# Performance work log

Measured on AMD Instinct MI355X. Metric: run time of the kernel, lower is better.

The kernel has to match this reference:

```python
import jax, jax.numpy as jnp
import numpy as np

DIM = 128
HOP = 2
NEIGH = [12, 2]  # neighbor_num per hop
ALPHA = 0.2      # leaky-relu slope
NUM_NODE = 50000
B, S = 128, 50
STDV = 1.0 / np.sqrt(DIM)


def _leaky(x):
    return jnp.where(x >= 0, x, ALPHA * x)


def _local_agg(h, adj, a_local):
    # h: [B,S,D], adj: [B,S,S] ints in 0..4, a_local: [4,D]
    a_in = h[:, :, None, :] * h[:, None, :, :]            # [B,S,S,D]
    e = _leaky(jnp.einsum('bijd,kd->kbij', a_in, a_local))  # [4,B,S,S]
    att = jnp.full(adj.shape, -9e15, dtype=h.dtype)
    for k in range(4):
        att = jnp.where(adj == k + 1, e[k], att)
    att = jax.nn.softmax(att, axis=-1)
    return jnp.einsum('bij,bjd->bid', att, h)


def _global_agg(self_v, neigh_v, extra_v, w1, w2, w3, bias):
    # self_v: [B,N,D], neigh_v: [B,N,K,D], extra_v: [B,N,D]
    a = _leaky(jnp.einsum('bnkd,de->bnke', extra_v[:, :, None, :] * neigh_v, w1))
    a = jnp.einsum('bnke,e->bnk', a, w2)
    a = jax.nn.softmax(a, axis=-1)
    agg = jnp.einsum('bnk,bnkd->bnd', a, neigh_v)
    out = jnp.concatenate([self_v, agg], axis=-1) @ w3 + bias
    return jax.nn.relu(out)


def setup_inputs() -> dict:
    key = jax.random.key(0)
    ks = jax.random.split(key, 12)
    u = lambda k, shp: jax.random.uniform(k, shp, jnp.float32, -STDV, STDV)
    return {
        'inputs': jax.random.randint(ks[0], (B, S), 0, NUM_NODE),
        'adj': jax.random.randint(ks[1], (B, S, S), 0, 5),
        'mask_item': jnp.ones((B, S), dtype=jnp.int32),
        'item': jax.random.randint(ks[2], (B, S), 0, NUM_NODE),
        'first_adj': jax.random.randint(ks[3], (B, S * NEIGH[0]), 0, NUM_NODE),
        'adj_all': jax.random.randint(ks[4], (NUM_NODE, 2), 0, NUM_NODE),
        'embedding': u(ks[5], (NUM_NODE, DIM)),
        'a_local': u(ks[6], (4, DIM)),
        'gw1': u(ks[7], (HOP, DIM, DIM)),
        'gw2': u(ks[8], (HOP, DIM)),
        'gw3': u(ks[9], (HOP, 2 * DIM, DIM)),
        'gbias': u(ks[10], (HOP, DIM)),
    }


def reference(inputs, adj, mask_item, item, first_adj, adj_all,
              embedding, a_local, gw1, gw2, gw3, gbias):
    b, s = inputs.shape
    h = embedding[inputs]                                  # [B,S,D]
    h_local = _local_agg(h, adj, a_local)

    m = mask_item.astype(embedding.dtype)[..., None]       # [B,S,1]
    item_emb = embedding[item] * m
    sum_item = jnp.sum(item_emb, 1) / jnp.sum(m, 1)        # [B,D]
    sess = sum_item[:, None, :]                            # [B,1,D]

    # multi-hop neighbor sampling
    neigh1 = first_adj.reshape(b, s * NEIGH[0])            # [B, 600]
    neigh2 = adj_all[neigh1.reshape(-1)].reshape(b, s * NEIGH[0] * NEIGH[1])  # [B,1200]
    ev = [embedding[inputs], embedding[neigh1], embedding[neigh2]]

    for n_hop in range(HOP):
        nxt = []
        for hop in range(HOP - n_hop):
            neigh_v = ev[hop + 1].reshape(b, -1, NEIGH[hop], DIM)
            extra_v = jnp.broadcast_to(sess, (b, ev[hop].shape[1], DIM))
            nxt.append(_global_agg(ev[hop], neigh_v, extra_v,
                                   gw1[n_hop], gw2[n_hop], gw3[n_hop], gbias[n_hop]))
        ev = nxt
    h_global = ev[0].reshape(b, s, DIM)

    # dropout is identity at eval
    return h_local + h_global
```

## Files before the change

kernel.cpp:

```cpp
#include <hip/hip_runtime.h>
#include <stdint.h>

typedef unsigned short ushort_t;
typedef __attribute__((ext_vector_type(8))) short bf16x8;
typedef __attribute__((ext_vector_type(4))) float f32x4;

#define B_   128
#define S_   50
#define D_   128
#define ALPHA_ 0.2f

__device__ __forceinline__ float bf2f(ushort_t u){
  return __uint_as_float(((uint32_t)u) << 16);
}
__device__ __forceinline__ ushort_t f2bf(float f){
  uint32_t x = __float_as_uint(f);
  x = (x + 0x7fffu + ((x >> 16) & 1u)) >> 16;
  return (ushort_t)x;
}
__device__ __forceinline__ float leaky(float x){ return x >= 0.f ? x : ALPHA_*x; }

__device__ __forceinline__ int detect_flag_block(const uint32_t* __restrict__ emb_raw){
  __shared__ int flg;
  if (threadIdx.x == 0){
    int ok = 1;
    for (int i = 0; i < 64; i++){
      uint32_t lo = emb_raw[i] & 0xffffu;
      uint32_t ex = (lo >> 7) & 0xFFu;
      if (!(lo == 0u || (ex >= 64u && ex <= 126u))) ok = 0;
    }
    flg = ok;
  }
  __syncthreads();
  return flg;
}

__global__ void cvt_all(const void* __restrict__ p0, const void* __restrict__ p1,
                        const void* __restrict__ p2, const void* __restrict__ p3,
                        const void* __restrict__ p4, const void* __restrict__ p5,
                        ushort_t* __restrict__ dst){
  int flag = detect_flag_block((const uint32_t*)p0);
  const int seg_end[6] = {6400000, 6400512, 6433280, 6433536, 6499072, 6499328};
  int base = (blockIdx.x*256 + threadIdx.x) * 4;
  if (base >= 6499328) return;
  int s = 0;
  while (base >= seg_end[s]) s++;
  int segbase = (s == 0) ? 0 : seg_end[s-1];
  const void* src = (s==0)?p0:(s==1)?p1:(s==2)?p2:(s==3)?p3:(s==4)?p4:p5;
  int off = base - segbase;
  union { ushort_t u[4]; uint2 d2; } o;
  if (flag){
    o.d2 = *(const uint2*)((const ushort_t*)src + off);
  } else {
    float4 v = *(const float4*)((const float*)src + off);
    o.u[0] = f2bf(v.x); o.u[1] = f2bf(v.y); o.u[2] = f2bf(v.z); o.u[3] = f2bf(v.w);
  }
  *(uint2*)(dst + base) = o.d2;
}

__global__ void prep_frags(const void* __restrict__ emb_raw,
                           const void* __restrict__ w1r, const void* __restrict__ w3r,
                           uint4* __restrict__ w1f, uint4* __restrict__ w3f){
  int flag = detect_flag_block((const uint32_t*)emb_raw);
  int id = blockIdx.x*256 + threadIdx.x;
  if (id >= 12288) return;
  if (id < 4096){
    int h = id >> 11, i = id & 2047;
    int kt = i >> 9, rem = i & 511, t = rem >> 6, ln = rem & 63;
    int q = ln >> 4, c = ln & 15;
    union { ushort_t u[8]; uint4 q4; } e;
    #pragma unroll
    for (int j = 0; j < 8; j++){
      int idx = h*16384 + (32*kt + q*8 + j)*128 + 16*t + c;
      e.u[j] = flag ? ((const ushort_t*)w1r)[idx] : f2bf(((const float*)w1r)[idx]);
    }
    w1f[h*2048 + i] = e.q4;
  } else {
    int id2 = id - 4096;
    int h = id2 >> 12, i = id2 & 4095;
    int kt = i >> 9, rem = i & 511, t = rem >> 6, ln = rem & 63;
    int q = ln >> 4, c = ln & 15;
    union { ushort_t u[8]; uint4 q4; } e;
    #pragma unroll
    for (int j = 0; j < 8; j++){
      int idx = h*32768 + (32*kt + q*8 + j)*128 + 16*t + c;
      e.u[j] = flag ? ((const ushort_t*)w3r)[idx] : f2bf(((const float*)w3r)[idx]);
    }
    w3f[h*4096 + i] = e.q4;
  }
}

__global__ __launch_bounds__(256) void sess_local(
    const int* __restrict__ inputs, const int* __restrict__ adj,
    const int* __restrict__ item, const int* __restrict__ mask,
    const ushort_t* __restrict__ emb, const ushort_t* __restrict__ alocb,
    ushort_t* __restrict__ sessb, ushort_t* __restrict__ hlb){
  int blk = blockIdx.x;
  int tid = threadIdx.x;
  if (blk >= 512){
    int b = (blk - 512)*2 + (tid >> 7);
    int d = tid & 127;
    float acc = 0.f, den = 0.f;
    for (int s = 0; s < S_; s++){
      float fm = (float)mask[b*S_ + s];
      int id = item[b*S_ + s];
      acc += fm * bf2f(emb[(size_t)id*D_ + d]);
      den += fm;
    }
    sessb[b*D_ + d] = f2bf(acc / den);
    return;
  }
  __shared__ ushort_t hS[64][136];
  __shared__ float    attS[16][68];
  __shared__ int      sids[64];
  int b  = blk >> 2;
  int mi = blk & 3;
  if (tid < 64) sids[tid] = (tid < S_) ? inputs[b*S_ + tid] : 0;
  __syncthreads();
  for (int idx = tid; idx < 64*16; idx += 256){
    int j = idx >> 4, ch = idx & 15;
    uint4 v = {0u, 0u, 0u, 0u};
    if (j < S_) v = *(const uint4*)(emb + (size_t)sids[j]*D_ + ch*8);
    *(uint4*)(&hS[j][ch*8]) = v;
  }
  for (int idx = tid; idx < 16*64; idx += 256)
    attS[idx >> 6][idx & 63] = -9.0e15f;
  __syncthreads();

  int lane = tid & 63, wv = tid >> 6;
  int q = lane >> 4, c = lane & 15;

  f32x4 Eacc[4];
  #pragma unroll
  for (int ni = 0; ni < 4; ni++) Eacc[ni] = (f32x4){0.f,0.f,0.f,0.f};
  #pragma unroll
  for (int kt = 0; kt < 4; kt++){
    uint4 av = *(const uint4*)(alocb + wv*D_ + kt*32 + q*8);
    const uint32_t* ap = (const uint32_t*)&av;
    uint4 hv = *(const uint4*)(&hS[mi*16 + c][kt*32 + q*8]);
    const uint32_t* hp = (const uint32_t*)&hv;
    union { ushort_t u[8]; bf16x8 v; } afr;
    #pragma unroll
    for (int p = 0; p < 4; p++){
      float x0 = __uint_as_float(hp[p] << 16)         * __uint_as_float(ap[p] << 16);
      float x1 = __uint_as_float(hp[p] & 0xffff0000u) * __uint_as_float(ap[p] & 0xffff0000u);
      afr.u[2*p]   = f2bf(x0);
      afr.u[2*p+1] = f2bf(x1);
    }
    #pragma unroll
    for (int ni = 0; ni < 4; ni++){
      union { uint4 q4; bf16x8 v; } bfr;
      bfr.q4 = *(const uint4*)(&hS[ni*16 + c][kt*32 + q*8]);
      Eacc[ni] = __builtin_amdgcn_mfma_f32_16x16x32_bf16(afr.v, bfr.v, Eacc[ni], 0,0,0);
    }
  }
  const int* adjb = adj + (size_t)b*S_*S_;
  #pragma unroll
  for (int ni = 0; ni < 4; ni++){
    int j = ni*16 + c;
    #pragma unroll
    for (int r = 0; r < 4; r++){
      int i = mi*16 + q*4 + r;
      if (i < S_ && j < S_){
        int kk = adjb[i*S_ + j];
        if (kk == wv + 1) attS[q*4 + r][j] = leaky(Eacc[ni][r]);
      }
    }
  }
  __syncthreads();
  if (tid < 16){
    int i = mi*16 + tid;
    if (i < S_){
      float mx = -__builtin_inff();
      for (int j = 0; j < S_; j++) mx = fmaxf(mx, attS[tid][j]);
      float s = 0.f;
      for (int j = 0; j < S_; j++){ float e = __expf(attS[tid][j] - mx); attS[tid][j] = e; s += e; }
      float inv = 1.f / s;
      for (int j = 0; j < S_; j++) attS[tid][j] *= inv;
      for (int j = S_; j < 64; j++) attS[tid][j] = 0.f;
    } else {
      for (int j = 0; j < 64; j++) attS[tid][j] = 0.f;
    }
  }
  __syncthreads();
  f32x4 Pacc[2];
  Pacc[0] = (f32x4){0.f,0.f,0.f,0.f};
  Pacc[1] = (f32x4){0.f,0.f,0.f,0.f};
  #pragma unroll
  for (int kt = 0; kt < 2; kt++){
    union { ushort_t u[8]; bf16x8 v; } afr;
    const float* arow = &attS[c][kt*32 + q*8];
    #pragma unroll
    for (int j = 0; j < 8; j++) afr.u[j] = f2bf(arow[j]);
    #pragma unroll
    for (int nn = 0; nn < 2; nn++){
      int ni = 2*wv + nn;
      union { ushort_t u[8]; bf16x8 v; } bfr;
      #pragma unroll
      for (int jj = 0; jj < 8; jj++)
        bfr.u[jj] = hS[kt*32 + q*8 + jj][ni*16 + c];
      Pacc[nn] = __builtin_amdgcn_mfma_f32_16x16x32_bf16(afr.v, bfr.v, Pacc[nn], 0,0,0);
    }
  }
  #pragma unroll
  for (int nn = 0; nn < 2; nn++){
    int d = (2*wv + nn)*16 + c;
    #pragma unroll
    for (int r = 0; r < 4; r++){
      int i = mi*16 + q*4 + r;
      if (i < S_) hlb[((size_t)b*S_ + i)*D_ + d] = f2bf(Pacc[nn][r]);
    }
  }
}

__global__ __launch_bounds__(256) void score_mfma_ab(
    const ushort_t* __restrict__ sessb, const ushort_t* __restrict__ emb,
    const int* __restrict__ neigh1, const int* __restrict__ adj_all,
    const uint4* __restrict__ w1f, const ushort_t* __restrict__ w2,
    float* __restrict__ score, int nA){
  __shared__ uint4 bfrag[2048];
  int tid = threadIdx.x;
  for (int i = tid; i < 2048; i += 256) bfrag[i] = w1f[i];
  __syncthreads();
  int lane = tid & 63, wave = tid >> 6;
  int m = lane & 15, q = lane >> 4;
  float w2v[8];
  #pragma unroll
  for (int t = 0; t < 8; t++) w2v[t] = bf2f(w2[16*t + m]);

  for (int it = 0; it < 2; it++){
    int row_base = blockIdx.x*128 + it*64 + wave*16;
    int row = row_base + m;
    const ushort_t* nrow; int b;
    if (row < nA){
      nrow = emb + (size_t)neigh1[row]*D_;
      b = row / 600;
    } else {
      int r2 = row - nA;
      nrow = emb + (size_t)adj_all[(size_t)neigh1[r2>>1]*2 + (r2&1)]*D_;
      b = r2 / 1200;
    }
    const ushort_t* srow = sessb + (size_t)b*D_;

    f32x4 acc[8];
    #pragma unroll
    for (int t = 0; t < 8; t++) acc[t] = (f32x4){0.f,0.f,0.f,0.f};
    #pragma unroll
    for (int kt = 0; kt < 4; kt++){
      uint4 nv = *(const uint4*)(nrow + kt*32 + q*8);
      uint4 sv = *(const uint4*)(srow + kt*32 + q*8);
      const uint32_t* np = (const uint32_t*)&nv;
      const uint32_t* sp = (const uint32_t*)&sv;
      union { ushort_t u[8]; bf16x8 v; } afr;
      #pragma unroll
      for (int p = 0; p < 4; p++){
        uint32_t n2 = np[p], s2 = sp[p];
        float a0 = __uint_as_float(n2 << 16)          * __uint_as_float(s2 << 16);
        float a1 = __uint_as_float(n2 & 0xffff0000u)  * __uint_as_float(s2 & 0xffff0000u);
        afr.u[2*p]   = f2bf(a0);
        afr.u[2*p+1] = f2bf(a1);
      }
      #pragma unroll
      for (int t = 0; t < 8; t++){
        union { uint4 q4; bf16x8 v; } bfr;
        bfr.q4 = bfrag[(kt*8 + t)*64 + lane];
        acc[t] = __builtin_amdgcn_mfma_f32_16x16x32_bf16(afr.v, bfr.v, acc[t], 0, 0, 0);
      }
    }
    #pragma unroll
    for (int r = 0; r < 4; r++){
      float s = 0.f;
      #pragma unroll
      for (int t = 0; t < 8; t++) s += leaky(acc[t][r]) * w2v[t];
      s += __shfl_xor(s, 1, 64);
      s += __shfl_xor(s, 2, 64);
      s += __shfl_xor(s, 4, 64);
      s += __shfl_xor(s, 8, 64);
      if (m == 0) score[row_base + q*4 + r] = s;
    }
  }
}

__global__ __launch_bounds__(256) void score_mfma_c(
    const ushort_t* __restrict__ sessb, const ushort_t* __restrict__ out1,
    const uint4* __restrict__ w1f, const ushort_t* __restrict__ w2,
    float* __restrict__ score){
  __shared__ uint4 bfrag[2048];
  int tid = threadIdx.x;
  for (int i = tid; i < 2048; i += 256) bfrag[i] = w1f[i];
  __syncthreads();
  int lane = tid & 63, wave = tid >> 6;
  int m = lane & 15, q = lane >> 4;
  float w2v[8];
  #pragma unroll
  for (int t = 0; t < 8; t++) w2v[t] = bf2f(w2[16*t + m]);
  for (int it = 0; it < 2; it++){
    int row_base = blockIdx.x*128 + it*64 + wave*16;
    int row = row_base + m;
    const ushort_t* nrow = out1 + (size_t)row*D_;
    int b = row / 600;
    const ushort_t* srow = sessb + (size_t)b*D_;
    f32x4 acc[8];
    #pragma unroll
    for (int t = 0; t < 8; t++) acc[t] = (f32x4){0.f,0.f,0.f,0.f};
    #pragma unroll
    for (int kt = 0; kt < 4; kt++){
      uint4 nv = *(const uint4*)(nrow + kt*32 + q*8);
      uint4 sv = *(const uint4*)(srow + kt*32 + q*8);
      const uint32_t* np = (const uint32_t*)&nv;
      const uint32_t* sp = (const uint32_t*)&sv;
      union { ushort_t u[8]; bf16x8 v; } afr;
      #pragma unroll
      for (int p = 0; p < 4; p++){
        uint32_t n2 = np[p], s2 = sp[p];
        float a0 = __uint_as_float(n2 << 16)          * __uint_as_float(s2 << 16);
        float a1 = __uint_as_float(n2 & 0xffff0000u)  * __uint_as_float(s2 & 0xffff0000u);
        afr.u[2*p]   = f2bf(a0);
        afr.u[2*p+1] = f2bf(a1);
      }
      #pragma unroll
      for (int t = 0; t < 8; t++){
        union { uint4 q4; bf16x8 v; } bfr;
        bfr.q4 = bfrag[(kt*8 + t)*64 + lane];
        acc[t] = __builtin_amdgcn_mfma_f32_16x16x32_bf16(afr.v, bfr.v, acc[t], 0, 0, 0);
      }
    }
    #pragma unroll
    for (int r = 0; r < 4; r++){
      float s = 0.f;
      #pragma unroll
      for (int t = 0; t < 8; t++) s += leaky(acc[t][r]) * w2v[t];
      s += __shfl_xor(s, 1, 64);
      s += __shfl_xor(s, 2, 64);
      s += __shfl_xor(s, 4, 64);
      s += __shfl_xor(s, 8, 64);
      if (m == 0) score[row_base + q*4 + r] = s;
    }
  }
}

template<int K>
__device__ __forceinline__ void softmaxK(const float* __restrict__ sc, float att[K]){
  float mx = -__builtin_inff();
  #pragma unroll
  for (int k = 0; k < K; k++){ att[k] = sc[k]; mx = fmaxf(mx, att[k]); }
  float s = 0.f;
  #pragma unroll
  for (int k = 0; k < K; k++){ att[k] = __expf(att[k] - mx); s += att[k]; }
  float inv = 1.f / s;
  #pragma unroll
  for (int k = 0; k < K; k++) att[k] *= inv;
}

template<int K>
__device__ __forceinline__ void out_tile(
    int lane, const uint4* __restrict__ afrag,
    const ushort_t* __restrict__ sptr, const ushort_t* const nptr[K],
    const float att[K], f32x4 acc[8]){
  int q = lane >> 4;
  #pragma unroll
  for (int kt = 0; kt < 8; kt++){
    union { ushort_t u[8]; uint4 q4; bf16x8 v; } bfr;
    if (kt < 4){
      bfr.q4 = *(const uint4*)(sptr + kt*32 + q*8);
    } else {
      float g[8] = {0,0,0,0,0,0,0,0};
      #pragma unroll
      for (int k = 0; k < K; k++){
        uint4 nv = *(const uint4*)(nptr[k] + (kt-4)*32 + q*8);
        const uint32_t* np = (const uint32_t*)&nv;
        #pragma unroll
        for (int p = 0; p < 4; p++){
          g[2*p]   = fmaf(att[k], __uint_as_float(np[p] << 16),         g[2*p]);
          g[2*p+1] = fmaf(att[k], __uint_as_float(np[p] & 0xffff0000u), g[2*p+1]);
        }
      }
      #pragma unroll
      for (int j = 0; j < 8; j++) bfr.u[j] = f2bf(g[j]);
    }
    #pragma unroll
    for (int t = 0; t < 8; t++){
      union { uint4 q4; bf16x8 v; } af;
      af.q4 = afrag[(kt*8 + t)*64 + lane];
      acc[t] = __builtin_amdgcn_mfma_f32_16x16x32_bf16(af.v, bfr.v, acc[t], 0, 0, 0);
    }
  }
}

__global__ __launch_bounds__(512) void out_mfma_ab(
    const float* __restrict__ score, const int* __restrict__ idx,
    const int* __restrict__ nbr, const int* __restrict__ adj_all,
    const ushort_t* __restrict__ emb, const uint4* __restrict__ w3f,
    const ushort_t* __restrict__ bias,
    ushort_t* __restrict__ o0c, ushort_t* __restrict__ out1c,
    int nA, int nTot, int scoreBbase){
  __shared__ uint4 afrag[4096];
  int tid = threadIdx.x;
  for (int i = tid; i < 4096; i += 512) afrag[i] = w3f[i];
  __syncthreads();
  int lane = tid & 63, wave = tid >> 6;
  int mrow = lane & 15, q = lane >> 4;
  float bv[8][4];
  #pragma unroll
  for (int t = 0; t < 8; t++){
    const ushort_t* bp = bias + 16*t + q*4;
    #pragma unroll
    for (int r = 0; r < 4; r++) bv[t][r] = bf2f(bp[r]);
  }
  int row_base = blockIdx.x*128 + wave*16;
  int row = row_base + mrow;
  bool active = row < nTot;
  int rowc = active ? row : (nTot - 1);
  bool isA = rowc < nA;
  f32x4 acc[8];
  #pragma unroll
  for (int t = 0; t < 8; t++) acc[t] = (f32x4){0.f,0.f,0.f,0.f};
  if (isA){
    const ushort_t* sptr = emb + (size_t)idx[rowc]*D_;
    const ushort_t* nptr[12];
    #pragma unroll
    for (int k = 0; k < 12; k++) nptr[k] = emb + (size_t)nbr[rowc*12 + k]*D_;
    float att[12];
    softmaxK<12>(score + (size_t)rowc*12, att);
    out_tile<12>(lane, afrag, sptr, nptr, att, acc);
  } else {
    int rB = rowc - nA;
    const ushort_t* sptr = emb + (size_t)nbr[rB]*D_;
    const ushort_t* nptr[2];
    #pragma unroll
    for (int k = 0; k < 2; k++) nptr[k] = emb + (size_t)adj_all[(size_t)nbr[rB]*2 + k]*D_;
    float att[2];
    softmaxK<2>(score + scoreBbase + (size_t)rB*2, att);
    out_tile<2>(lane, afrag, sptr, nptr, att, acc);
  }
  if (active){
    ushort_t* dst = isA ? (o0c + (size_t)row*D_) : (out1c + (size_t)(row - nA)*D_);
    #pragma unroll
    for (int t = 0; t < 8; t++){
      int col0 = 16*t + q*4;
      union { ushort_t u[4]; uint2 d2; } pk;
      #pragma unroll
      for (int r = 0; r < 4; r++) pk.u[r] = f2bf(fmaxf(acc[t][r] + bv[t][r], 0.f));
      *(uint2*)(dst + col0) = pk.d2;
    }
  }
}

__global__ __launch_bounds__(512) void out_mfma_c(
    const float* __restrict__ score, const ushort_t* __restrict__ out1,
    const ushort_t* __restrict__ selfsrc, const uint4* __restrict__ w3f,
    const ushort_t* __restrict__ bias,
    const ushort_t* __restrict__ addsrc, float* __restrict__ outf, int nrows){
  __shared__ uint4 afrag[4096];
  int tid = threadIdx.x;
  for (int i = tid; i < 4096; i += 512) afrag[i] = w3f[i];
  __syncthreads();
  int lane = tid & 63, wave = tid >> 6;
  int mrow = lane & 15, q = lane >> 4;
  float bv[8][4];
  #pragma unroll
  for (int t = 0; t < 8; t++){
    const ushort_t* bp = bias + 16*t + q*4;
    #pragma unroll
    for (int r = 0; r < 4; r++) bv[t][r] = bf2f(bp[r]);
  }
  int row_base = blockIdx.x*128 + wave*16;
  int row = row_base + mrow;
  bool active = row < nrows;
  int rowc = active ? row : (nrows - 1);
  const ushort_t* sptr = selfsrc + (size_t)rowc*D_;
  const ushort_t* nptr[12];
  #pragma unroll
  for (int k = 0; k < 12; k++) nptr[k] = out1 + (size_t)(rowc*12 + k)*D_;
  float att[12];
  softmaxK<12>(score + (size_t)rowc*12, att);
  f32x4 acc[8];
  #pragma unroll
  for (int t = 0; t < 8; t++) acc[t] = (f32x4){0.f,0.f,0.f,0.f};
  out_tile<12>(lane, afrag, sptr, nptr, att, acc);
  if (active){
    #pragma unroll
    for (int t = 0; t < 8; t++){
      int col0 = 16*t + q*4;
      float v[4];
      const ushort_t* ap = addsrc + (size_t)row*D_ + col0;
      #pragma unroll
      for (int r = 0; r < 4; r++)
        v[r] = fmaxf(acc[t][r] + bv[t][r], 0.f) + bf2f(ap[r]);
      *(f32x4*)(outf + (size_t)row*D_ + col0) = (f32x4){v[0], v[1], v[2], v[3]};
    }
  }
}

extern "C" void kernel_launch(void* const* d_in, const int* in_sizes, int n_in,
                              void* d_out, int out_size, void* d_ws, size_t ws_size,
                              hipStream_t stream) {
  const int* inputs    = (const int*)d_in[0];
  const int* adj       = (const int*)d_in[1];
  const int* mask_item = (const int*)d_in[2];
  const int* item      = (const int*)d_in[3];
  const int* first_adj = (const int*)d_in[4];
  const int* adj_all   = (const int*)d_in[5];

  char* ws = (char*)d_ws;
  size_t o = 0;
  ushort_t* emb_b  = (ushort_t*)(ws + o); o += 12800000;
  ushort_t* alocb  = (ushort_t*)(ws + o); o += 1024;
  ushort_t* gw1b   = (ushort_t*)(ws + o); o += 65536;
  ushort_t* gw2b   = (ushort_t*)(ws + o); o += 512;
  ushort_t* gw3b   = (ushort_t*)(ws + o); o += 131072;
  ushort_t* gbb    = (ushort_t*)(ws + o); o += 512;
  ushort_t* sessb  = (ushort_t*)(ws + o); o += 32768;
  ushort_t* hlb    = (ushort_t*)(ws + o); o += 1638400;
  uint4*    w1f    = (uint4*)(ws + o);    o += 65536;
  uint4*    w3f    = (uint4*)(ws + o);    o += 131072;
  size_t fixed = o;
  (void)gw1b; (void)gw3b;
  int CHB = 16;
  if      (ws_size >= fixed + (size_t)128*173600) CHB = 128;
  else if (ws_size >= fixed + (size_t)64 *173600) CHB = 64;
  else if (ws_size >= fixed + (size_t)32 *173600) CHB = 32;
  ushort_t* out1c = (ushort_t*)(ws + o);  o += (size_t)CHB*153600;
  ushort_t* o0c   = (ushort_t*)(ws + o);  o += (size_t)CHB*12800;
  float*    score = (float*)(ws + o);

  float* outp = (float*)d_out;

  cvt_all<<<(6499328/4 + 255)/256, 256, 0, stream>>>(d_in[6], d_in[7], d_in[8], d_in[9],
                                                     d_in[10], d_in[11], emb_b);
  prep_frags<<<48, 256, 0, stream>>>(d_in[6], d_in[8], d_in[10], w1f, w3f);

  sess_local<<<576, 256, 0, stream>>>(inputs, adj, item, mask_item,
                                      emb_b, alocb, sessb, hlb);

  int nchunk = B_ / CHB;
  for (int c = 0; c < nchunk; c++){
    int b0 = c * CHB;
    const int* fadj  = first_adj + (size_t)b0 * 600;
    const ushort_t* sbc = sessb + (size_t)b0 * D_;
    ushort_t*  hlc   = hlb  + (size_t)b0 * 50 * D_;
    float*     outc  = outp + (size_t)b0 * 50 * D_;
    int nA600 = CHB*600, nA50 = CHB*50, nTot = CHB*650;

    score_mfma_ab<<<(3*nA600)/128, 256, 0, stream>>>(sbc, emb_b, fadj, adj_all,
                                                     w1f, gw2b, score, nA600);
    out_mfma_ab<<<(nTot + 127)/128, 512, 0, stream>>>(score, inputs + b0*50, fadj, adj_all,
                                                      emb_b, w3f, gbb, o0c, out1c,
                                                      nA50, nTot, nA600);
    score_mfma_c<<<nA600/128, 256, 0, stream>>>(sbc, out1c, w1f + 2048, gw2b + 128, score);
    out_mfma_c<<<(nA50 + 127)/128, 512, 0, stream>>>(score, out1c, o0c,
                                                     w3f + 4096, gbb + 128,
                                                     hlc, outc, nA50);
  }
}
```

Measured before the change: 199.4 us.

## Fuse prep kernels into one launch and fuse score with output aggregation

The conversion, weight-fragment prep and session/local-attention kernels become one launch, with block ranges picking the role. The local and session paths now read the raw embedding directly instead of waiting for the converted copy. Each hop's score kernel is folded into its output kernel: scores for a block's rows are computed into LDS, then the W3 fragments are reloaded into the same buffer, which removes the global score buffer and two launches per chunk. The local softmax is also spread across 16 lanes per row instead of one thread per row, at the cost of extra LDS reloads and a larger, more complex kernel.

```diff
diff --git a/kernel.cpp b/kernel.cpp
--- a/kernel.cpp
+++ b/kernel.cpp
@@ -35,307 +35,262 @@
   return flg;
 }
 
-__global__ void cvt_all(const void* __restrict__ p0, const void* __restrict__ p1,
-                        const void* __restrict__ p2, const void* __restrict__ p3,
-                        const void* __restrict__ p4, const void* __restrict__ p5,
-                        ushort_t* __restrict__ dst){
-  int flag = detect_flag_block((const uint32_t*)p0);
-  const int seg_end[6] = {6400000, 6400512, 6433280, 6433536, 6499072, 6499328};
-  int base = (blockIdx.x*256 + threadIdx.x) * 4;
-  if (base >= 6499328) return;
-  int s = 0;
-  while (base >= seg_end[s]) s++;
-  int segbase = (s == 0) ? 0 : seg_end[s-1];
-  const void* src = (s==0)?p0:(s==1)?p1:(s==2)?p2:(s==3)?p3:(s==4)?p4:p5;
-  int off = base - segbase;
-  union { ushort_t u[4]; uint2 d2; } o;
-  if (flag){
-    o.d2 = *(const uint2*)((const ushort_t*)src + off);
-  } else {
-    float4 v = *(const float4*)((const float*)src + off);
-    o.u[0] = f2bf(v.x); o.u[1] = f2bf(v.y); o.u[2] = f2bf(v.z); o.u[3] = f2bf(v.w);
-  }
-  *(uint2*)(dst + base) = o.d2;
-}
-
-__global__ void prep_frags(const void* __restrict__ emb_raw,
-                           const void* __restrict__ w1r, const void* __restrict__ w3r,
-                           uint4* __restrict__ w1f, uint4* __restrict__ w3f){
-  int flag = detect_flag_block((const uint32_t*)emb_raw);
-  int id = blockIdx.x*256 + threadIdx.x;
-  if (id >= 12288) return;
-  if (id < 4096){
-    int h = id >> 11, i = id & 2047;
-    int kt = i >> 9, rem = i & 511, t = rem >> 6, ln = rem & 63;
-    int q = ln >> 4, c = ln & 15;
-    union { ushort_t u[8]; uint4 q4; } e;
-    #pragma unroll
-    for (int j = 0; j < 8; j++){
-      int idx = h*16384 + (32*kt + q*8 + j)*128 + 16*t + c;
-      e.u[j] = flag ? ((const ushort_t*)w1r)[idx] : f2bf(((const float*)w1r)[idx]);
-    }
-    w1f[h*2048 + i] = e.q4;
-  } else {
-    int id2 = id - 4096;
-    int h = id2 >> 12, i = id2 & 4095;
-    int kt = i >> 9, rem = i & 511, t = rem >> 6, ln = rem & 63;
-    int q = ln >> 4, c = ln & 15;
-    union { ushort_t u[8]; uint4 q4; } e;
-    #pragma unroll
-    for (int j = 0; j < 8; j++){
-      int idx = h*32768 + (32*kt + q*8 + j)*128 + 16*t + c;
-      e.u[j] = flag ? ((const ushort_t*)w3r)[idx] : f2bf(((const float*)w3r)[idx]);
-    }
-    w3f[h*4096 + i] = e.q4;
-  }
-}
-
-__global__ __launch_bounds__(256) void sess_local(
+#define NLOCAL_ 512
+#define NSESS_  64
+#define NCVT_   6347
+#define NPREP_  48
+
+__global__ __launch_bounds__(256) void k1(
     const int* __restrict__ inputs, const int* __restrict__ adj,
     const int* __restrict__ item, const int* __restrict__ mask,
-    const ushort_t* __restrict__ emb, const ushort_t* __restrict__ alocb,
-    ushort_t* __restrict__ sessb, ushort_t* __restrict__ hlb){
-  int blk = blockIdx.x;
-  int tid = threadIdx.x;
-  if (blk >= 512){
-    int b = (blk - 512)*2 + (tid >> 7);
+    const void* __restrict__ p0, const void* __restrict__ p1,
+    const void* __restrict__ p2, const void* __restrict__ p3,
+    const void* __restrict__ p4, const void* __restrict__ p5,
+    ushort_t* __restrict__ emb_b, uint4* __restrict__ w1f, uint4* __restrict__ w3f,
+    ushort_t* __restrict__ sessb, ushort_t* __restrict__ hlb)
+{
+  int blk = blockIdx.x, tid = threadIdx.x;
+  int flag = detect_flag_block((const uint32_t*)p0);
+
+  if (blk < NLOCAL_){
+    __shared__ ushort_t hS[64][136];
+    __shared__ float    attS[16][68];
+    __shared__ int      sids[64];
+    __shared__ ushort_t alS[512];
+    int b  = blk >> 2;
+    int mi = blk & 3;
+    if (tid < 64) sids[tid] = (tid < S_) ? inputs[b*S_ + tid] : 0;
+    for (int i = tid; i < 512; i += 256)
+      alS[i] = flag ? ((const ushort_t*)p1)[i] : f2bf(((const float*)p1)[i]);
+    __syncthreads();
+    if (flag){
+      const ushort_t* e16 = (const ushort_t*)p0;
+      for (int idx = tid; idx < 64*16; idx += 256){
+        int j = idx >> 4, ch = idx & 15;
+        uint4 v = {0u, 0u, 0u, 0u};
+        if (j < S_) v = *(const uint4*)(e16 + (size_t)sids[j]*D_ + ch*8);
+        *(uint4*)(&hS[j][ch*8]) = v;
+      }
+    } else {
+      const float* ef = (const float*)p0;
+      for (int idx = tid; idx < 64*32; idx += 256){
+        int j = idx >> 5, ch = idx & 31;
+        union { ushort_t u[4]; uint2 d2; } o;
+        o.d2 = make_uint2(0u, 0u);
+        if (j < S_){
+          float4 v = *(const float4*)(ef + (size_t)sids[j]*D_ + ch*4);
+          o.u[0]=f2bf(v.x); o.u[1]=f2bf(v.y); o.u[2]=f2bf(v.z); o.u[3]=f2bf(v.w);
+        }
+        *(uint2*)(&hS[j][ch*4]) = o.d2;
+      }
+    }
+    for (int idx = tid; idx < 16*64; idx += 256)
+      attS[idx >> 6][idx & 63] = -9.0e15f;
+    __syncthreads();
+
+    int lane = tid & 63, wv = tid >> 6;
+    int q = lane >> 4, c = lane & 15;
+
+    f32x4 Eacc[4];
+    #pragma unroll
+    for (int ni = 0; ni < 4; ni++) Eacc[ni] = (f32x4){0.f,0.f,0.f,0.f};
+    #pragma unroll
+    for (int kt = 0; kt < 4; kt++){
+      uint4 av = *(const uint4*)(alS + wv*D_ + kt*32 + q*8);
+      const uint32_t* ap = (const uint32_t*)&av;
+      uint4 hv = *(const uint4*)(&hS[mi*16 + c][kt*32 + q*8]);
+      const uint32_t* hp = (const uint32_t*)&hv;
+      union { ushort_t u[8]; bf16x8 v; } afr;
+      #pragma unroll
+      for (int p = 0; p < 4; p++){
+        float x0 = __uint_as_float(hp[p] << 16)         * __uint_as_float(ap[p] << 16);
+        float x1 = __uint_as_float(hp[p] & 0xffff0000u) * __uint_as_float(ap[p] & 0xffff0000u);
+        afr.u[2*p]   = f2bf(x0);
+        afr.u[2*p+1] = f2bf(x1);
+      }
+      #pragma unroll
+      for (int ni = 0; ni < 4; ni++){
+        union { uint4 q4; bf16x8 v; } bfr;
+        bfr.q4 = *(const uint4*)(&hS[ni*16 + c][kt*32 + q*8]);
+        Eacc[ni] = __builtin_amdgcn_mfma_f32_16x16x32_bf16(afr.v, bfr.v, Eacc[ni], 0,0,0);
+      }
+    }
+    const int* adjb = adj + (size_t)b*S_*S_;
+    #pragma unroll
+    for (int ni = 0; ni < 4; ni++){
+      int j = ni*16 + c;
+      #pragma unroll
+      for (int r = 0; r < 4; r++){
+        int i = mi*16 + q*4 + r;
+        if (i < S_ && j < S_){
+          int kk = adjb[i*S_ + j];
+          if (kk == wv + 1) attS[q*4 + r][j] = leaky(Eacc[ni][r]);
+        }
+      }
+    }
+    __syncthreads();
+    {
+      int r  = tid >> 4;
+      int cg = tid & 15;
+      int i  = mi*16 + r;
+      float v0 = attS[r][cg*4+0], v1 = attS[r][cg*4+1];
+      float v2 = attS[r][cg*4+2], v3 = attS[r][cg*4+3];
+      float mx = fmaxf(fmaxf(v0,v1), fmaxf(v2,v3));
+      #pragma unroll
+      for (int off = 1; off < 16; off <<= 1) mx = fmaxf(mx, __shfl_xor(mx, off, 16));
+      float e0 = (cg*4+0 < S_) ? __expf(v0 - mx) : 0.f;
+      float e1 = (cg*4+1 < S_) ? __expf(v1 - mx) : 0.f;
+      float e2 = (cg*4+2 < S_) ? __expf(v2 - mx) : 0.f;
+      float e3 = (cg*4+3 < S_) ? __expf(v3 - mx) : 0.f;
+      float s = e0 + e1 + e2 + e3;
+      #pragma unroll
+      for (int off = 1; off < 16; off <<= 1) s += __shfl_xor(s, off, 16);
+      float inv = (i < S_) ? 1.f / s : 0.f;
+      attS[r][cg*4+0] = e0*inv;
+      attS[r][cg*4+1] = e1*inv;
+      attS[r][cg*4+2] = e2*inv;
+      attS[r][cg*4+3] = e3*inv;
+    }
+    __syncthreads();
+    f32x4 Pacc[2];
+    Pacc[0] = (f32x4){0.f,0.f,0.f,0.f};
+    Pacc[1] = (f32x4){0.f,0.f,0.f,0.f};
+    #pragma unroll
+    for (int kt = 0; kt < 2; kt++){
+      union { ushort_t u[8]; bf16x8 v; } afr;
+      const float* arow = &attS[c][kt*32 + q*8];
+      #pragma unroll
+      for (int j = 0; j < 8; j++) afr.u[j] = f2bf(arow[j]);
+      #pragma unroll
+      for (int nn = 0; nn < 2; nn++){
+        int ni = 2*wv + nn;
+        union { ushort_t u[8]; bf16x8 v; } bfr;
+        #pragma unroll
+        for (int jj = 0; jj < 8; jj++)
+          bfr.u[jj] = hS[kt*32 + q*8 + jj][ni*16 + c];
+        Pacc[nn] = __builtin_amdgcn_mfma_f32_16x16x32_bf16(afr.v, bfr.v, Pacc[nn], 0,0,0);
+      }
+    }
+    #pragma unroll
+    for (int nn = 0; nn < 2; nn++){
+      int d = (2*wv + nn)*16 + c;
+      #pragma unroll
+      for (int r = 0; r < 4; r++){
+        int i = mi*16 + q*4 + r;
+        if (i < S_) hlb[((size_t)b*S_ + i)*D_ + d] = f2bf(Pacc[nn][r]);
+      }
+    }
+  } else if (blk < NLOCAL_ + NSESS_){
+    int b = (blk - NLOCAL_)*2 + (tid >> 7);
     int d = tid & 127;
     float acc = 0.f, den = 0.f;
-    for (int s = 0; s < S_; s++){
-      float fm = (float)mask[b*S_ + s];
-      int id = item[b*S_ + s];
-      acc += fm * bf2f(emb[(size_t)id*D_ + d]);
-      den += fm;
+    if (flag){
+      const ushort_t* e16 = (const ushort_t*)p0;
+      for (int s = 0; s < S_; s++){
+        float fm = (float)mask[b*S_ + s];
+        int id = item[b*S_ + s];
+        acc += fm * bf2f(e16[(size_t)id*D_ + d]);
+        den += fm;
+      }
+    } else {
+      const float* ef = (const float*)p0;
+      for (int s = 0; s < S_; s++){
+        float fm = (float)mask[b*S_ + s];
+        int id = item[b*S_ + s];
+        acc += fm * ef[(size_t)id*D_ + d];
+        den += fm;
+      }
     }
     sessb[b*D_ + d] = f2bf(acc / den);
-    return;
-  }
-  __shared__ ushort_t hS[64][136];
-  __shared__ float    attS[16][68];
-  __shared__ int      sids[64];
-  int b  = blk >> 2;
-  int mi = blk & 3;
-  if (tid < 64) sids[tid] = (tid < S_) ? inputs[b*S_ + tid] : 0;
-  __syncthreads();
-  for (int idx = tid; idx < 64*16; idx += 256){
-    int j = idx >> 4, ch = idx & 15;
-    uint4 v = {0u, 0u, 0u, 0u};
-    if (j < S_) v = *(const uint4*)(emb + (size_t)sids[j]*D_ + ch*8);
-    *(uint4*)(&hS[j][ch*8]) = v;
-  }
-  for (int idx = tid; idx < 16*64; idx += 256)
-    attS[idx >> 6][idx & 63] = -9.0e15f;
-  __syncthreads();
-
-  int lane = tid & 63, wv = tid >> 6;
-  int q = lane >> 4, c = lane & 15;
-
-  f32x4 Eacc[4];
-  #pragma unroll
-  for (int ni = 0; ni < 4; ni++) Eacc[ni] = (f32x4){0.f,0.f,0.f,0.f};
+  } else if (blk < NLOCAL_ + NSESS_ + NCVT_){
+    const int seg_end[6] = {6400000, 6400512, 6433280, 6433536, 6499072, 6499328};
+    int base = ((blk - NLOCAL_ - NSESS_)*256 + tid) * 4;
+    if (base >= 6499328) return;
+    int s = 0;
+    while (base >= seg_end[s]) s++;
+    int segbase = (s == 0) ? 0 : seg_end[s-1];
+    const void* src = (s==0)?p0:(s==1)?p1:(s==2)?p2:(s==3)?p3:(s==4)?p4:p5;
+    int off = base - segbase;
+    union { ushort_t u[4]; uint2 d2; } o;
+    if (flag){
+      o.d2 = *(const uint2*)((const ushort_t*)src + off);
+    } else {
+      float4 v = *(const float4*)((const float*)src + off);
+      o.u[0] = f2bf(v.x); o.u[1] = f2bf(v.y); o.u[2] = f2bf(v.z); o.u[3] = f2bf(v.w);
+    }
+    *(uint2*)(emb_b + base) = o.d2;
+  } else {
+    int id = (blk - NLOCAL_ - NSESS_ - NCVT_)*256 + tid;
+    if (id >= 12288) return;
+    if (id < 4096){
+      int h = id >> 11, i = id & 2047;
+      int kt = i >> 9, rem = i & 511, t = rem >> 6, ln = rem & 63;
+      int q = ln >> 4, c = ln & 15;
+      union { ushort_t u[8]; uint4 q4; } e;
+      #pragma unroll
+      for (int j = 0; j < 8; j++){
+        int idx = h*16384 + (32*kt + q*8 + j)*128 + 16*t + c;
+        e.u[j] = flag ? ((const ushort_t*)p2)[idx] : f2bf(((const float*)p2)[idx]);
+      }
+      w1f[h*2048 + i] = e.q4;
+    } else {
+      int id2 = id - 4096;
+      int h = id2 >> 12, i = id2 & 4095;
+      int kt = i >> 9, rem = i & 511, t = rem >> 6, ln = rem & 63;
+      int q = ln >> 4, c = ln & 15;
+      union { ushort_t u[8]; uint4 q4; } e;
+      #pragma unroll
+      for (int j = 0; j < 8; j++){
+        int idx = h*32768 + (32*kt + q*8 + j)*128 + 16*t + c;
+        e.u[j] = flag ? ((const ushort_t*)p4)[idx] : f2bf(((const float*)p4)[idx]);
+      }
+      w3f[h*4096 + i] = e.q4;
+    }
+  }
+}
+
+
+__device__ __forceinline__ void score_tile16(
+    int lane, const uint4* __restrict__ bfrag,
+    const ushort_t* __restrict__ nrow, const ushort_t* __restrict__ srow,
+    const float* __restrict__ w2v, float sv[4])
+{
+  int q = lane >> 4;
+  f32x4 acc[8];
+  #pragma unroll
+  for (int t = 0; t < 8; t++) acc[t] = (f32x4){0.f,0.f,0.f,0.f};
   #pragma unroll
   for (int kt = 0; kt < 4; kt++){
-    uint4 av = *(const uint4*)(alocb + wv*D_ + kt*32 + q*8);
-    const uint32_t* ap = (const uint32_t*)&av;
-    uint4 hv = *(const uint4*)(&hS[mi*16 + c][kt*32 + q*8]);
-    const uint32_t* hp = (const uint32_t*)&hv;
+    uint4 nv = *(const uint4*)(nrow + kt*32 + q*8);
+    uint4 svv = *(const uint4*)(srow + kt*32 + q*8);
+    const uint32_t* np = (const uint32_t*)&nv;
+    const uint32_t* sp = (const uint32_t*)&svv;
     union { ushort_t u[8]; bf16x8 v; } afr;
     #pragma unroll
     for (int p = 0; p < 4; p++){
-      float x0 = __uint_as_float(hp[p] << 16)         * __uint_as_float(ap[p] << 16);
-      float x1 = __uint_as_float(hp[p] & 0xffff0000u) * __uint_as_float(ap[p] & 0xffff0000u);
-      afr.u[2*p]   = f2bf(x0);
-      afr.u[2*p+1] = f2bf(x1);
-    }
-    #pragma unroll
-    for (int ni = 0; ni < 4; ni++){
+      uint32_t n2 = np[p], s2 = sp[p];
+      float a0 = __uint_as_float(n2 << 16)          * __uint_as_float(s2 << 16);
+      float a1 = __uint_as_float(n2 & 0xffff0000u)  * __uint_as_float(s2 & 0xffff0000u);
+      afr.u[2*p]   = f2bf(a0);
+      afr.u[2*p+1] = f2bf(a1);
+    }
+    #pragma unroll
+    for (int t = 0; t < 8; t++){
       union { uint4 q4; bf16x8 v; } bfr;
-      bfr.q4 = *(const uint4*)(&hS[ni*16 + c][kt*32 + q*8]);
-      Eacc[ni] = __builtin_amdgcn_mfma_f32_16x16x32_bf16(afr.v, bfr.v, Eacc[ni], 0,0,0);
-    }
-  }
-  const int* adjb = adj + (size_t)b*S_*S_;
-  #pragma unroll
-  for (int ni = 0; ni < 4; ni++){
-    int j = ni*16 + c;
-    #pragma unroll
-    for (int r = 0; r < 4; r++){
-      int i = mi*16 + q*4 + r;
-      if (i < S_ && j < S_){
-        int kk = adjb[i*S_ + j];
-        if (kk == wv + 1) attS[q*4 + r][j] = leaky(Eacc[ni][r]);
-      }
-    }
-  }
-  __syncthreads();
-  if (tid < 16){
-    int i = mi*16 + tid;
-    if (i < S_){
-      float mx = -__builtin_inff();
-      for (int j = 0; j < S_; j++) mx = fmaxf(mx, attS[tid][j]);
-      float s = 0.f;
-      for (int j = 0; j < S_; j++){ float e = __expf(attS[tid][j] - mx); attS[tid][j] = e; s += e; }
-      float inv = 1.f / s;
-      for (int j = 0; j < S_; j++) attS[tid][j] *= inv;
-      for (int j = S_; j < 64; j++) attS[tid][j] = 0.f;
-    } else {
-      for (int j = 0; j < 64; j++) attS[tid][j] = 0.f;
-    }
-  }
-  __syncthreads();
-  f32x4 Pacc[2];
-  Pacc[0] = (f32x4){0.f,0.f,0.f,0.f};
-  Pacc[1] = (f32x4){0.f,0.f,0.f,0.f};
-  #pragma unroll
-  for (int kt = 0; kt < 2; kt++){
-    union { ushort_t u[8]; bf16x8 v; } afr;
-    const float* arow = &attS[c][kt*32 + q*8];
-    #pragma unroll
-    for (int j = 0; j < 8; j++) afr.u[j] = f2bf(arow[j]);
-    #pragma unroll
-    for (int nn = 0; nn < 2; nn++){
-      int ni = 2*wv + nn;
-      union { ushort_t u[8]; bf16x8 v; } bfr;
-      #pragma unroll
-      for (int jj = 0; jj < 8; jj++)
-        bfr.u[jj] = hS[kt*32 + q*8 + jj][ni*16 + c];
-      Pacc[nn] = __builtin_amdgcn_mfma_f32_16x16x32_bf16(afr.v, bfr.v, Pacc[nn], 0,0,0);
-    }
-  }
-  #pragma unroll
-  for (int nn = 0; nn < 2; nn++){
-    int d = (2*wv + nn)*16 + c;
-    #pragma unroll
-    for (int r = 0; r < 4; r++){
-      int i = mi*16 + q*4 + r;
-      if (i < S_) hlb[((size_t)b*S_ + i)*D_ + d] = f2bf(Pacc[nn][r]);
-    }
-  }
-}
-
-__global__ __launch_bounds__(256) void score_mfma_ab(
-    const ushort_t* __restrict__ sessb, const ushort_t* __restrict__ emb,
-    const int* __restrict__ neigh1, const int* __restrict__ adj_all,
-    const uint4* __restrict__ w1f, const ushort_t* __restrict__ w2,
-    float* __restrict__ score, int nA){
-  __shared__ uint4 bfrag[2048];
-  int tid = threadIdx.x;
-  for (int i = tid; i < 2048; i += 256) bfrag[i] = w1f[i];
-  __syncthreads();
-  int lane = tid & 63, wave = tid >> 6;
-  int m = lane & 15, q = lane >> 4;
-  float w2v[8];
-  #pragma unroll
-  for (int t = 0; t < 8; t++) w2v[t] = bf2f(w2[16*t + m]);
-
-  for (int it = 0; it < 2; it++){
-    int row_base = blockIdx.x*128 + it*64 + wave*16;
-    int row = row_base + m;
-    const ushort_t* nrow; int b;
-    if (row < nA){
-      nrow = emb + (size_t)neigh1[row]*D_;
-      b = row / 600;
-    } else {
-      int r2 = row - nA;
-      nrow = emb + (size_t)adj_all[(size_t)neigh1[r2>>1]*2 + (r2&1)]*D_;
-      b = r2 / 1200;
-    }
-    const ushort_t* srow = sessb + (size_t)b*D_;
-
-    f32x4 acc[8];
-    #pragma unroll
-    for (int t = 0; t < 8; t++) acc[t] = (f32x4){0.f,0.f,0.f,0.f};
-    #pragma unroll
-    for (int kt = 0; kt < 4; kt++){
-      uint4 nv = *(const uint4*)(nrow + kt*32 + q*8);
-      uint4 sv = *(const uint4*)(srow + kt*32 + q*8);
-      const uint32_t* np = (const uint32_t*)&nv;
-      const uint32_t* sp = (const uint32_t*)&sv;
-      union { ushort_t u[8]; bf16x8 v; } afr;
-      #pragma unroll
-      for (int p = 0; p < 4; p++){
-        uint32_t n2 = np[p], s2 = sp[p];
-        float a0 = __uint_as_float(n2 << 16)          * __uint_as_float(s2 << 16);
-        float a1 = __uint_as_float(n2 & 0xffff0000u)  * __uint_as_float(s2 & 0xffff0000u);
-        afr.u[2*p]   = f2bf(a0);
-        afr.u[2*p+1] = f2bf(a1);
-      }
-      #pragma unroll
-      for (int t = 0; t < 8; t++){
-        union { uint4 q4; bf16x8 v; } bfr;
-        bfr.q4 = bfrag[(kt*8 + t)*64 + lane];
-        acc[t] = __builtin_amdgcn_mfma_f32_16x16x32_bf16(afr.v, bfr.v, acc[t], 0, 0, 0);
-      }
-    }
-    #pragma unroll
-    for (int r = 0; r < 4; r++){
-      float s = 0.f;
-      #pragma unroll
-      for (int t = 0; t < 8; t++) s += leaky(acc[t][r]) * w2v[t];
-      s += __shfl_xor(s, 1, 64);
-      s += __shfl_xor(s, 2, 64);
-      s += __shfl_xor(s, 4, 64);
-      s += __shfl_xor(s, 8, 64);
-      if (m == 0) score[row_base + q*4 + r] = s;
-    }
-  }
-}
-
-__global__ __launch_bounds__(256) void score_mfma_c(
-    const ushort_t* __restrict__ sessb, const ushort_t* __restrict__ out1,
-    const uint4* __restrict__ w1f, const ushort_t* __restrict__ w2,
-    float* __restrict__ score){
-  __shared__ uint4 bfrag[2048];
-  int tid = threadIdx.x;
-  for (int i = tid; i < 2048; i += 256) bfrag[i] = w1f[i];
-  __syncthreads();
-  int lane = tid & 63, wave = tid >> 6;
-  int m = lane & 15, q = lane >> 4;
-  float w2v[8];
-  #pragma unroll
-  for (int t = 0; t < 8; t++) w2v[t] = bf2f(w2[16*t + m]);
-  for (int it = 0; it < 2; it++){
-    int row_base = blockIdx.x*128 + it*64 + wave*16;
-    int row = row_base + m;
-    const ushort_t* nrow = out1 + (size_t)row*D_;
-    int b = row / 600;
-    const ushort_t* srow = sessb + (size_t)b*D_;
-    f32x4 acc[8];
-    #pragma unroll
-    for (int t = 0; t < 8; t++) acc[t] = (f32x4){0.f,0.f,0.f,0.f};
-    #pragma unroll
-    for (int kt = 0; kt < 4; kt++){
-      uint4 nv = *(const uint4*)(nrow + kt*32 + q*8);
-      uint4 sv = *(const uint4*)(srow + kt*32 + q*8);
-      const uint32_t* np = (const uint32_t*)&nv;
-      const uint32_t* sp = (const uint32_t*)&sv;
-      union { ushort_t u[8]; bf16x8 v; } afr;
-      #pragma unroll
-      for (int p = 0; p < 4; p++){
-        uint32_t n2 = np[p], s2 = sp[p];
-        float a0 = __uint_as_float(n2 << 16)          * __uint_as_float(s2 << 16);
-        float a1 = __uint_as_float(n2 & 0xffff0000u)  * __uint_as_float(s2 & 0xffff0000u);
-        afr.u[2*p]   = f2bf(a0);
-        afr.u[2*p+1] = f2bf(a1);
-      }
-      #pragma unroll
-      for (int t = 0; t < 8; t++){
-        union { uint4 q4; bf16x8 v; } bfr;
-        bfr.q4 = bfrag[(kt*8 + t)*64 + lane];
-        acc[t] = __builtin_amdgcn_mfma_f32_16x16x32_bf16(afr.v, bfr.v, acc[t], 0, 0, 0);
-      }
-    }
-    #pragma unroll
-    for (int r = 0; r < 4; r++){
-      float s = 0.f;
-      #pragma unroll
-      for (int t = 0; t < 8; t++) s += leaky(acc[t][r]) * w2v[t];
-      s += __shfl_xor(s, 1, 64);
-      s += __shfl_xor(s, 2, 64);
-      s += __shfl_xor(s, 4, 64);
-      s += __shfl_xor(s, 8, 64);
-      if (m == 0) score[row_base + q*4 + r] = s;
-    }
+      bfr.q4 = bfrag[(kt*8 + t)*64 + lane];
+      acc[t] = __builtin_amdgcn_mfma_f32_16x16x32_bf16(afr.v, bfr.v, acc[t], 0, 0, 0);
+    }
+  }
+  #pragma unroll
+  for (int r = 0; r < 4; r++){
+    float s = 0.f;
+    #pragma unroll
+    for (int t = 0; t < 8; t++) s += leaky(acc[t][r]) * w2v[t];
+    s += __shfl_xor(s, 1, 64);
+    s += __shfl_xor(s, 2, 64);
+    s += __shfl_xor(s, 4, 64);
+    s += __shfl_xor(s, 8, 64);
+    sv[r] = s;
   }
 }
 
@@ -387,19 +342,69 @@
   }
 }
 
-__global__ __launch_bounds__(512) void out_mfma_ab(
-    const float* __restrict__ score, const int* __restrict__ idx,
-    const int* __restrict__ nbr, const int* __restrict__ adj_all,
-    const ushort_t* __restrict__ emb, const uint4* __restrict__ w3f,
-    const ushort_t* __restrict__ bias,
+__global__ __launch_bounds__(512) void fused_ab(
+    const int* __restrict__ idx, const int* __restrict__ nbr,
+    const int* __restrict__ adj_all,
+    const ushort_t* __restrict__ sessb, const ushort_t* __restrict__ emb,
+    const uint4* __restrict__ w1f, const ushort_t* __restrict__ w2,
+    const uint4* __restrict__ w3f, const ushort_t* __restrict__ bias,
     ushort_t* __restrict__ o0c, ushort_t* __restrict__ out1c,
-    int nA, int nTot, int scoreBbase){
-  __shared__ uint4 afrag[4096];
+    int nA50, int nTot)
+{
+  __shared__ uint4 frag[4096];
+  __shared__ float attS[128][12];
   int tid = threadIdx.x;
-  for (int i = tid; i < 4096; i += 512) afrag[i] = w3f[i];
+  for (int i = tid; i < 2048; i += 512) frag[i] = w1f[i];
   __syncthreads();
   int lane = tid & 63, wave = tid >> 6;
-  int mrow = lane & 15, q = lane >> 4;
+  int m = lane & 15, q = lane >> 4;
+
+  int rb0   = blockIdx.x * 128;
+  int rows  = min(128, nTot - rb0);
+  int a_cnt = min(rows, max(0, nA50 - rb0));
+  int b_cnt = rows - a_cnt;
+  int athr  = a_cnt * 12;
+  int cnt   = athr + b_cnt * 2;
+  int tiles = (cnt + 15) >> 4;
+  int baseB2 = (rb0 + a_cnt - nA50) * 2;
+
+  {
+    float w2v[8];
+    #pragma unroll
+    for (int t = 0; t < 8; t++) w2v[t] = bf2f(w2[16*t + m]);
+    for (int t = wave; t < tiles; t += 8){
+      int ls = t*16 + m;
+      if (ls > cnt - 1) ls = cnt - 1;
+      const ushort_t* nrow; int b;
+      if (ls < athr){
+        int srow = rb0*12 + ls;
+        nrow = emb + (size_t)nbr[srow] * D_;
+        b = srow / 600;
+      } else {
+        int r2 = baseB2 + (ls - athr);
+        nrow = emb + (size_t)adj_all[(size_t)nbr[r2 >> 1]*2 + (r2 & 1)] * D_;
+        b = r2 / 1200;
+      }
+      float sv[4];
+      score_tile16(lane, frag, nrow, sessb + (size_t)b*D_, w2v, sv);
+      if (m == 0){
+        #pragma unroll
+        for (int r = 0; r < 4; r++){
+          int ls2 = t*16 + q*4 + r;
+          if (ls2 < cnt){
+            int lo, k;
+            if (ls2 < athr){ lo = ls2 / 12; k = ls2 - lo*12; }
+            else { int z = ls2 - athr; lo = a_cnt + (z >> 1); k = z & 1; }
+            attS[lo][k] = sv[r];
+          }
+        }
+      }
+    }
+  }
+  __syncthreads();
+  for (int i = tid; i < 4096; i += 512) frag[i] = w3f[i];
+  __syncthreads();
+
   float bv[8][4];
   #pragma unroll
   for (int t = 0; t < 8; t++){
@@ -407,11 +412,12 @@
     #pragma unroll
     for (int r = 0; r < 4; r++) bv[t][r] = bf2f(bp[r]);
   }
-  int row_base = blockIdx.x*128 + wave*16;
-  int row = row_base + mrow;
+  int row_base = rb0 + wave*16;
+  int row = row_base + m;
   bool active = row < nTot;
   int rowc = active ? row : (nTot - 1);
-  bool isA = rowc < nA;
+  bool isA = rowc < nA50;
+  int lo = rowc - rb0;
   f32x4 acc[8];
   #pragma unroll
   for (int t = 0; t < 8; t++) acc[t] = (f32x4){0.f,0.f,0.f,0.f};
@@ -421,20 +427,20 @@
     #pragma unroll
     for (int k = 0; k < 12; k++) nptr[k] = emb + (size_t)nbr[rowc*12 + k]*D_;
     float att[12];
-    softmaxK<12>(score + (size_t)rowc*12, att);
-    out_tile<12>(lane, afrag, sptr, nptr, att, acc);
+    softmaxK<12>(&attS[lo][0], att);
+    out_tile<12>(lane, frag, sptr, nptr, att, acc);
   } else {
-    int rB = rowc - nA;
+    int rB = rowc - nA50;
     const ushort_t* sptr = emb + (size_t)nbr[rB]*D_;
     const ushort_t* nptr[2];
     #pragma unroll
     for (int k = 0; k < 2; k++) nptr[k] = emb + (size_t)adj_all[(size_t)nbr[rB]*2 + k]*D_;
     float att[2];
-    softmaxK<2>(score + scoreBbase + (size_t)rB*2, att);
-    out_tile<2>(lane, afrag, sptr, nptr, att, acc);
+    softmaxK<2>(&attS[lo][0], att);
+    out_tile<2>(lane, frag, sptr, nptr, att, acc);
   }
   if (active){
-    ushort_t* dst = isA ? (o0c + (size_t)row*D_) : (out1c + (size_t)(row - nA)*D_);
+    ushort_t* dst = isA ? (o0c + (size_t)row*D_) : (out1c + (size_t)(row - nA50)*D_);
     #pragma unroll
     for (int t = 0; t < 8; t++){
       int col0 = 16*t + q*4;
@@ -446,17 +452,53 @@
   }
 }
 
-__global__ __launch_bounds__(512) void out_mfma_c(
-    const float* __restrict__ score, const ushort_t* __restrict__ out1,
-    const ushort_t* __restrict__ selfsrc, const uint4* __restrict__ w3f,
-    const ushort_t* __restrict__ bias,
-    const ushort_t* __restrict__ addsrc, float* __restrict__ outf, int nrows){
-  __shared__ uint4 afrag[4096];
+__global__ __launch_bounds__(512) void fused_c(
+    const ushort_t* __restrict__ sessb, const ushort_t* __restrict__ out1,
+    const ushort_t* __restrict__ selfsrc,
+    const uint4* __restrict__ w1f, const ushort_t* __restrict__ w2,
+    const uint4* __restrict__ w3f, const ushort_t* __restrict__ bias,
+    const ushort_t* __restrict__ addsrc, float* __restrict__ outf, int nrows)
+{
+  __shared__ uint4 frag[4096];
+  __shared__ float attS[128][12];
   int tid = threadIdx.x;
-  for (int i = tid; i < 4096; i += 512) afrag[i] = w3f[i];
+  for (int i = tid; i < 2048; i += 512) frag[i] = w1f[i];
   __syncthreads();
   int lane = tid & 63, wave = tid >> 6;
-  int mrow = lane & 15, q = lane >> 4;
+  int m = lane & 15, q = lane >> 4;
+
+  int rb0   = blockIdx.x * 128;
+  int rows  = min(128, nrows - rb0);
+  int cnt   = rows * 12;
+  int tiles = (cnt + 15) >> 4;
+  {
+    float w2v[8];
+    #pragma unroll
+    for (int t = 0; t < 8; t++) w2v[t] = bf2f(w2[16*t + m]);
+    for (int t = wave; t < tiles; t += 8){
+      int ls = t*16 + m;
+      if (ls > cnt - 1) ls = cnt - 1;
+      int srow = rb0*12 + ls;
+      const ushort_t* nrow = out1 + (size_t)srow*D_;
+      int b = srow / 600;
+      float sv[4];
+      score_tile16(lane, frag, nrow, sessb + (size_t)b*D_, w2v, sv);
+      if (m == 0){
+        #pragma unroll
+        for (int r = 0; r < 4; r++){
+          int ls2 = t*16 + q*4 + r;
+          if (ls2 < cnt){
+            int lo = ls2 / 12;
+            attS[lo][ls2 - lo*12] = sv[r];
+          }
+        }
+      }
+    }
+  }
+  __syncthreads();
+  for (int i = tid; i < 4096; i += 512) frag[i] = w3f[i];
+  __syncthreads();
+
   float bv[8][4];
   #pragma unroll
   for (int t = 0; t < 8; t++){
@@ -464,20 +506,20 @@
     #pragma unroll
     for (int r = 0; r < 4; r++) bv[t][r] = bf2f(bp[r]);
   }
-  int row_base = blockIdx.x*128 + wave*16;
-  int row = row_base + mrow;
+  int row = rb0 + wave*16 + m;
   bool active = row < nrows;
   int rowc = active ? row : (nrows - 1);
+  int lo = rowc - rb0;
   const ushort_t* sptr = selfsrc + (size_t)rowc*D_;
   const ushort_t* nptr[12];
   #pragma unroll
   for (int k = 0; k < 12; k++) nptr[k] = out1 + (size_t)(rowc*12 + k)*D_;
   float att[12];
-  softmaxK<12>(score + (size_t)rowc*12, att);
+  softmaxK<12>(&attS[lo][0], att);
   f32x4 acc[8];
   #pragma unroll
   for (int t = 0; t < 8; t++) acc[t] = (f32x4){0.f,0.f,0.f,0.f};
-  out_tile<12>(lane, afrag, sptr, nptr, att, acc);
+  out_tile<12>(lane, frag, sptr, nptr, att, acc);
   if (active){
     #pragma unroll
     for (int t = 0; t < 8; t++){
@@ -515,23 +557,20 @@
   uint4*    w1f    = (uint4*)(ws + o);    o += 65536;
   uint4*    w3f    = (uint4*)(ws + o);    o += 131072;
   size_t fixed = o;
-  (void)gw1b; (void)gw3b;
+  (void)alocb; (void)gw1b; (void)gw3b;
   int CHB = 16;
-  if      (ws_size >= fixed + (size_t)128*173600) CHB = 128;
-  else if (ws_size >= fixed + (size_t)64 *173600) CHB = 64;
-  else if (ws_size >= fixed + (size_t)32 *173600) CHB = 32;
+  if      (ws_size >= fixed + (size_t)128*166400) CHB = 128;
+  else if (ws_size >= fixed + (size_t)64 *166400) CHB = 64;
+  else if (ws_size >= fixed + (size_t)32 *166400) CHB = 32;
   ushort_t* out1c = (ushort_t*)(ws + o);  o += (size_t)CHB*153600;
   ushort_t* o0c   = (ushort_t*)(ws + o);  o += (size_t)CHB*12800;
-  float*    score = (float*)(ws + o);
 
   float* outp = (float*)d_out;
 
-  cvt_all<<<(6499328/4 + 255)/256, 256, 0, stream>>>(d_in[6], d_in[7], d_in[8], d_in[9],
-                                                     d_in[10], d_in[11], emb_b);
-  prep_frags<<<48, 256, 0, stream>>>(d_in[6], d_in[8], d_in[10], w1f, w3f);
-
-  sess_local<<<576, 256, 0, stream>>>(inputs, adj, item, mask_item,
-                                      emb_b, alocb, sessb, hlb);
+  k1<<<NLOCAL_ + NSESS_ + NCVT_ + NPREP_, 256, 0, stream>>>(
+      inputs, adj, item, mask_item,
+      d_in[6], d_in[7], d_in[8], d_in[9], d_in[10], d_in[11],
+      emb_b, w1f, w3f, sessb, hlb);
 
   int nchunk = B_ / CHB;
   for (int c = 0; c < nchunk; c++){
@@ -540,16 +579,14 @@
     const ushort_t* sbc = sessb + (size_t)b0 * D_;
     ushort_t*  hlc   = hlb  + (size_t)b0 * 50 * D_;
     float*     outc  = outp + (size_t)b0 * 50 * D_;
-    int nA600 = CHB*600, nA50 = CHB*50, nTot = CHB*650;
-
-    score_mfma_ab<<<(3*nA600)/128, 256, 0, stream>>>(sbc, emb_b, fadj, adj_all,
-                                                     w1f, gw2b, score, nA600);
-    out_mfma_ab<<<(nTot + 127)/128, 512, 0, stream>>>(score, inputs + b0*50, fadj, adj_all,
-                                                      emb_b, w3f, gbb, o0c, out1c,
-                                                      nA50, nTot, nA600);
-    score_mfma_c<<<nA600/128, 256, 0, stream>>>(sbc, out1c, w1f + 2048, gw2b + 128, score);
-    out_mfma_c<<<(nA50 + 127)/128, 512, 0, stream>>>(score, out1c, o0c,
-                                                     w3f + 4096, gbb + 128,
-                                                     hlc, outc, nA50);
-  }
-}
+    int nA50 = CHB*50, nTot = CHB*650;
+
+    fused_ab<<<(nTot + 127)/128, 512, 0, stream>>>(
+        inputs + b0*50, fadj, adj_all, sbc, emb_b,
+        w1f, gw2b, w3f, gbb, o0c, out1c, nA50, nTot);
+
+    fused_c<<<(nA50 + 127)/128, 512, 0, stream>>>(
+        sbc, out1c, o0c, w1f + 2048, gw2b + 128, w3f + 4096, gbb + 128,
+        hlc, outc, nA50);
+  }
+}
```

New measurement: 208.2 us. 4.4% more time.
